# Kernel tuning notes

Measured on AMD Instinct MI355X. Metric: run time of the kernel, lower is better.

The kernel has to match this reference:

```python
import jax, jax.numpy as jnp
import numpy as np

PATCH_SIZE = 32
HALF = PATCH_SIZE // 2


def setup_inputs() -> dict:
    key = jax.random.key(0)
    k1, k2 = jax.random.split(key)
    B, L, H, W = 64, 106, 512, 512
    img = jax.random.normal(k1, (B, 1, H, W), dtype=jnp.float32)
    # landmarks are (x, y) pixel coords; uniform over the image
    landmarks = jax.random.uniform(k2, (B, L, 2), dtype=jnp.float32,
                                   minval=0.0, maxval=float(H - 1))
    return {"img": img, "landmarks": landmarks}


def reference(img, landmarks):
    B = landmarks.shape[0]
    H, W = img.shape[2], img.shape[3]
    # integer offset grid, K = (2*HALF+1)^2 entries of (o0, o1)
    r = jnp.arange(-HALF, HALF + 1, dtype=jnp.int32)
    oy, ox = jnp.meshgrid(r, r, indexing="ij")
    offsets = jnp.stack([oy.reshape(-1), ox.reshape(-1)], axis=-1)  # [K, 2] int32
    offsets_f = offsets.astype(jnp.float32)

    lm = jnp.clip(landmarks.reshape(B, -1, 2), float(HALF), float(H - 1 - HALF))  # [B,L,2]
    lm_long = jnp.floor(lm)  # coords are >= 0 so trunc == floor, matches .long()

    # integer pixel locations per (landmark, offset): [B, K, L, 2]
    loc = offsets[None, :, None, :] + lm_long[:, None, :, :].astype(jnp.int32)
    flat_idx = (loc[..., 0] + loc[..., 1] * W).reshape(B, -1)  # [B, K*L]

    # subpixel residual and splat weights
    dxdy = lm - lm_long  # [B, L, 2]
    sub = offsets_f[None, :, None, :] - dxdy[:, None, :, :]  # [B, K, L, 2]
    vals = (1.0 / (1.0 + jnp.sqrt(jnp.sum(sub * sub, axis=-1) + 1e-6))).reshape(B, -1)

    out = jnp.zeros((B, H * W), dtype=jnp.float32)
    out = out.at[jnp.arange(B)[:, None], flat_idx].add(vals)
    return out.reshape(B, 1, H, W)
```

## Files before the change

kernel.cpp:

```cpp
#include <hip/hip_runtime.h>

#define HALF 16
#define IMW  512
#define IMH  512
#define TILE 32
#define TPA  16
#define TPI  256
#define MAXL 256

typedef float f32x4 __attribute__((ext_vector_type(4)));

__global__ __launch_bounds__(256)
void lm_gather_kernel(const float* __restrict__ landmarks,
                      float* __restrict__ out,
                      int L)
{
    __shared__ float2 slm[MAXL];
    __shared__ int sn;

    const int t    = threadIdx.x;
    const int bx   = blockIdx.x;
    const int b    = bx >> 8;
    const int tile = bx & (TPI - 1);
    const int tx   = tile & (TPA - 1);
    const int ty   = tile >> 4;

    if (t == 0) sn = 0;
    __syncthreads();

    const float2* lmb = reinterpret_cast<const float2*>(landmarks) + (size_t)b * L;
    for (int j = t; j < L; j += 256) {
        float2 lm = lmb[j];
        float x0 = fminf(fmaxf(lm.x, (float)HALF), (float)(IMW - 1 - HALF));
        float x1 = fminf(fmaxf(lm.y, (float)HALF), (float)(IMH - 1 - HALF));
        int i0 = (int)x0;
        int i1 = (int)x1;
        int tx0 = (i0 - HALF) >> 5;
        int ty0 = (i1 - HALF) >> 5;
        if ((unsigned)(tx - tx0) <= 1u && (unsigned)(ty - ty0) <= 1u) {
            int pos = atomicAdd(&sn, 1);
            if (pos < MAXL) slm[pos] = make_float2(x0, x1);
        }
    }
    __syncthreads();
    const int n = min(sn, MAXL);

    const int py  = ty * TILE + (t >> 3);
    const int px0 = tx * TILE + (t & 7) * 4;
    const float fpy = (float)py;

    float acc[4] = {0.0f, 0.0f, 0.0f, 0.0f};
    for (int j = 0; j < n; ++j) {
        float2 e = slm[j];
        int   i0   = (int)e.x;
        int   i1   = (int)e.y;
        float dy   = fpy - e.y;
        float dy2e = dy * dy + 1e-6f;
        bool  in1  = (unsigned)(py - i1 + HALF) <= (unsigned)(2 * HALF);
        #pragma unroll
        for (int c = 0; c < 4; ++c) {
            int   px  = px0 + c;
            float dx  = (float)px - e.x;
            bool  in0 = (unsigned)(px - i0 + HALF) <= (unsigned)(2 * HALF);
            float v = __builtin_amdgcn_rcpf(1.0f + __builtin_amdgcn_sqrtf(dx * dx + dy2e));
            acc[c] += (in0 && in1) ? v : 0.0f;
        }
    }

    float* op = out + (size_t)b * (IMH * IMW) + (size_t)py * IMW + px0;
    f32x4 v4 = { acc[0], acc[1], acc[2], acc[3] };
    __builtin_nontemporal_store(v4, reinterpret_cast<f32x4*>(op));
}

extern "C" void kernel_launch(void* const* d_in, const int* in_sizes, int n_in,
                              void* d_out, int out_size, void* d_ws, size_t ws_size,
                              hipStream_t stream)
{
    const float* landmarks = (const float*)d_in[1];
    float* out = (float*)d_out;

    const int B = out_size / (IMH * IMW);
    const int L = in_sizes[1] / (2 * B);

    lm_gather_kernel<<<B * TPI, 256, 0, stream>>>(landmarks, out, L);
}
```

Baseline: 23.69 us.

## Process full-width row strips per block with binned landmarks and LDS-staged stores

Each block now handles a 32-row strip of the image instead of a 32x32 tile. Landmarks are scanned once per strip and binned into 16 column sub-tile lists, and results are staged in a 64KB shared buffer before being written out as contiguous rows. This aims to cut redundant landmark scanning and block-launch overhead. In exchange, occupancy is lower because of the large LDS use, the grid is much smaller, and compute is serialized before stores.

```diff
diff --git a/kernel.cpp b/kernel.cpp
--- a/kernel.cpp
+++ b/kernel.cpp
@@ -1,31 +1,31 @@
 #include <hip/hip_runtime.h>
 
-#define HALF 16
-#define IMW  512
-#define IMH  512
-#define TILE 32
-#define TPA  16
-#define TPI  256
-#define MAXL 256
+#define HALF   16
+#define IMW    512
+#define IMH    512
+#define SH     32
+#define NSTRIP (IMH / SH)
+#define NSUB   16
+#define CAP    64
 
 typedef float f32x4 __attribute__((ext_vector_type(4)));
 
 __global__ __launch_bounds__(256)
-void lm_gather_kernel(const float* __restrict__ landmarks,
-                      float* __restrict__ out,
-                      int L)
+void lm_strip_kernel(const float* __restrict__ landmarks,
+                     float* __restrict__ out,
+                     int L)
 {
-    __shared__ float2 slm[MAXL];
-    __shared__ int sn;
+    __shared__ float  sbuf[SH][IMW];
+    __shared__ float2 slist[NSUB][CAP];
+    __shared__ int    scnt[NSUB];
 
-    const int t    = threadIdx.x;
-    const int bx   = blockIdx.x;
-    const int b    = bx >> 8;
-    const int tile = bx & (TPI - 1);
-    const int tx   = tile & (TPA - 1);
-    const int ty   = tile >> 4;
+    const int t  = threadIdx.x;
+    const int bx = blockIdx.x;
+    const int b  = bx >> 4;
+    const int ty = bx & (NSTRIP - 1);
+    const int R  = ty * SH;
 
-    if (t == 0) sn = 0;
+    if (t < NSUB) scnt[t] = 0;
     __syncthreads();
 
     const float2* lmb = reinterpret_cast<const float2*>(landmarks) + (size_t)b * L;
@@ -35,41 +35,56 @@
         float x1 = fminf(fmaxf(lm.y, (float)HALF), (float)(IMH - 1 - HALF));
         int i0 = (int)x0;
         int i1 = (int)x1;
-        int tx0 = (i0 - HALF) >> 5;
-        int ty0 = (i1 - HALF) >> 5;
-        if ((unsigned)(tx - tx0) <= 1u && (unsigned)(ty - ty0) <= 1u) {
-            int pos = atomicAdd(&sn, 1);
-            if (pos < MAXL) slm[pos] = make_float2(x0, x1);
+        if ((unsigned)(i1 - (R - HALF)) < (unsigned)(SH + 2 * HALF)) {
+            int sx0 = (i0 - HALF) >> 5;
+            int sx1 = (i0 + HALF) >> 5;
+            int p0 = atomicAdd(&scnt[sx0], 1);
+            if (p0 < CAP) slist[sx0][p0] = make_float2(x0, x1);
+            if (sx1 != sx0) {
+                int p1 = atomicAdd(&scnt[sx1], 1);
+                if (p1 < CAP) slist[sx1][p1] = make_float2(x0, x1);
+            }
         }
     }
     __syncthreads();
-    const int n = min(sn, MAXL);
 
-    const int py  = ty * TILE + (t >> 3);
-    const int px0 = tx * TILE + (t & 7) * 4;
+    const int   r   = t >> 3;
+    const int   c0  = (t & 7) * 4;
+    const int   py  = R + r;
     const float fpy = (float)py;
 
-    float acc[4] = {0.0f, 0.0f, 0.0f, 0.0f};
-    for (int j = 0; j < n; ++j) {
-        float2 e = slm[j];
-        int   i0   = (int)e.x;
-        int   i1   = (int)e.y;
-        float dy   = fpy - e.y;
-        float dy2e = dy * dy + 1e-6f;
-        bool  in1  = (unsigned)(py - i1 + HALF) <= (unsigned)(2 * HALF);
-        #pragma unroll
-        for (int c = 0; c < 4; ++c) {
-            int   px  = px0 + c;
-            float dx  = (float)px - e.x;
-            bool  in0 = (unsigned)(px - i0 + HALF) <= (unsigned)(2 * HALF);
-            float v = __builtin_amdgcn_rcpf(1.0f + __builtin_amdgcn_sqrtf(dx * dx + dy2e));
-            acc[c] += (in0 && in1) ? v : 0.0f;
+    for (int tx = 0; tx < NSUB; ++tx) {
+        const int n   = min(scnt[tx], CAP);
+        const int px0 = tx * 32 + c0;
+        float acc[4] = {0.0f, 0.0f, 0.0f, 0.0f};
+        for (int j = 0; j < n; ++j) {
+            float2 e = slist[tx][j];
+            int   i0   = (int)e.x;
+            int   i1   = (int)e.y;
+            float dy   = fpy - e.y;
+            float dy2e = dy * dy + 1e-6f;
+            bool  in1  = (unsigned)(py - i1 + HALF) <= (unsigned)(2 * HALF);
+            #pragma unroll
+            for (int c = 0; c < 4; ++c) {
+                int   px  = px0 + c;
+                float dx  = (float)px - e.x;
+                bool  in0 = (unsigned)(px - i0 + HALF) <= (unsigned)(2 * HALF);
+                float v = __builtin_amdgcn_rcpf(1.0f + __builtin_amdgcn_sqrtf(dx * dx + dy2e));
+                acc[c] += (in0 && in1) ? v : 0.0f;
+            }
         }
+        f32x4 v4 = { acc[0], acc[1], acc[2], acc[3] };
+        *reinterpret_cast<f32x4*>(&sbuf[r][px0]) = v4;
     }
+    __syncthreads();
 
-    float* op = out + (size_t)b * (IMH * IMW) + (size_t)py * IMW + px0;
-    f32x4 v4 = { acc[0], acc[1], acc[2], acc[3] };
-    __builtin_nontemporal_store(v4, reinterpret_cast<f32x4*>(op));
+    float*       op = out + (size_t)b * (IMH * IMW) + (size_t)R * IMW;
+    const float* sp = &sbuf[0][0];
+    #pragma unroll
+    for (int s = 0; s < 16; ++s) {
+        f32x4 v = *reinterpret_cast<const f32x4*>(sp + s * 1024 + t * 4);
+        __builtin_nontemporal_store(v, reinterpret_cast<f32x4*>(op + s * 1024 + t * 4));
+    }
 }
 
 extern "C" void kernel_launch(void* const* d_in, const int* in_sizes, int n_in,
@@ -82,5 +97,5 @@
     const int B = out_size / (IMH * IMW);
     const int L = in_sizes[1] / (2 * B);
 
-    lm_gather_kernel<<<B * TPI, 256, 0, stream>>>(landmarks, out, L);
+    lm_strip_kernel<<<B * NSTRIP, 256, 0, stream>>>(landmarks, out, L);
 }
```

Measured after the change: 28.56 us. +20.6%, slower.

## Pre-bin landmarks per tile in a separate kernel before per-tile gather

Applied to the files above, without the earlier changes.

Adds a binning kernel, one block per image, that atomically appends each clamped landmark to the four 32x32 tile lists it can touch. The stored lists live in workspace with a per-tile cap of 48. The gather kernel then reads only its tile's short list instead of every block scanning all L landmarks and running a shared-memory atomic filter. It also replaces the nontemporal output store with a plain vector store. The cost is a second launch, a global-memory round trip, and a fixed cap: dense clusters past 48 entries would be silently truncated, where the old cap was 256.

```diff
diff --git a/kernel.cpp b/kernel.cpp
--- a/kernel.cpp
+++ b/kernel.cpp
@@ -3,55 +3,64 @@
 #define HALF 16
 #define IMW  512
 #define IMH  512
-#define TILE 32
-#define TPA  16
+#define TSZ  32
+#define NT   16
 #define TPI  256
-#define MAXL 256
+#define CAP  48
 
 typedef float f32x4 __attribute__((ext_vector_type(4)));
 
 __global__ __launch_bounds__(256)
-void lm_gather_kernel(const float* __restrict__ landmarks,
-                      float* __restrict__ out,
-                      int L)
+void lm_bin_kernel(const float* __restrict__ landmarks, int L,
+                   int* __restrict__ cnt, float2* __restrict__ lists)
 {
-    __shared__ float2 slm[MAXL];
-    __shared__ int sn;
-
-    const int t    = threadIdx.x;
-    const int bx   = blockIdx.x;
-    const int b    = bx >> 8;
-    const int tile = bx & (TPI - 1);
-    const int tx   = tile & (TPA - 1);
-    const int ty   = tile >> 4;
-
-    if (t == 0) sn = 0;
+    const int b = blockIdx.x;
+    const int t = threadIdx.x;
+    int* c = cnt + b * TPI;
+    if (t < TPI) c[t] = 0;
     __syncthreads();
-
-    const float2* lmb = reinterpret_cast<const float2*>(landmarks) + (size_t)b * L;
-    for (int j = t; j < L; j += 256) {
-        float2 lm = lmb[j];
+    if (t < L) {
+        float2 lm = reinterpret_cast<const float2*>(landmarks)[(size_t)b * L + t];
         float x0 = fminf(fmaxf(lm.x, (float)HALF), (float)(IMW - 1 - HALF));
         float x1 = fminf(fmaxf(lm.y, (float)HALF), (float)(IMH - 1 - HALF));
         int i0 = (int)x0;
         int i1 = (int)x1;
         int tx0 = (i0 - HALF) >> 5;
         int ty0 = (i1 - HALF) >> 5;
-        if ((unsigned)(tx - tx0) <= 1u && (unsigned)(ty - ty0) <= 1u) {
-            int pos = atomicAdd(&sn, 1);
-            if (pos < MAXL) slm[pos] = make_float2(x0, x1);
-        }
+        #pragma unroll
+        for (int dy = 0; dy < 2; ++dy)
+            #pragma unroll
+            for (int dx = 0; dx < 2; ++dx) {
+                int tile = (ty0 + dy) * NT + (tx0 + dx);
+                int pos = atomicAdd(&c[tile], 1);
+                if (pos < CAP)
+                    lists[((size_t)b * TPI + tile) * CAP + pos] = make_float2(x0, x1);
+            }
     }
-    __syncthreads();
-    const int n = min(sn, MAXL);
+}
 
-    const int py  = ty * TILE + (t >> 3);
-    const int px0 = tx * TILE + (t & 7) * 4;
+__global__ __launch_bounds__(256)
+void lm_gather_kernel(const int* __restrict__ cnt,
+                      const float2* __restrict__ lists,
+                      float* __restrict__ out)
+{
+    const int bx   = blockIdx.x;
+    const int b    = bx >> 8;
+    const int tile = bx & (TPI - 1);
+    const int tx   = tile & (NT - 1);
+    const int ty   = tile >> 4;
+
+    const int     n   = min(cnt[bx], CAP);
+    const float2* lst = lists + (size_t)bx * CAP;
+
+    const int   t   = threadIdx.x;
+    const int   py  = ty * TSZ + (t >> 3);
+    const int   px0 = tx * TSZ + (t & 7) * 4;
     const float fpy = (float)py;
 
     float acc[4] = {0.0f, 0.0f, 0.0f, 0.0f};
     for (int j = 0; j < n; ++j) {
-        float2 e = slm[j];
+        float2 e = lst[j];
         int   i0   = (int)e.x;
         int   i1   = (int)e.y;
         float dy   = fpy - e.y;
@@ -69,7 +78,7 @@
 
     float* op = out + (size_t)b * (IMH * IMW) + (size_t)py * IMW + px0;
     f32x4 v4 = { acc[0], acc[1], acc[2], acc[3] };
-    __builtin_nontemporal_store(v4, reinterpret_cast<f32x4*>(op));
+    *reinterpret_cast<f32x4*>(op) = v4;
 }
 
 extern "C" void kernel_launch(void* const* d_in, const int* in_sizes, int n_in,
@@ -82,5 +91,9 @@
     const int B = out_size / (IMH * IMW);
     const int L = in_sizes[1] / (2 * B);
 
-    lm_gather_kernel<<<B * TPI, 256, 0, stream>>>(landmarks, out, L);
+    int*    cnt   = (int*)d_ws;
+    float2* lists = (float2*)((char*)d_ws + (size_t)B * TPI * sizeof(int));
+
+    lm_bin_kernel<<<B, 256, 0, stream>>>(landmarks, L, cnt, lists);
+    lm_gather_kernel<<<B * TPI, 256, 0, stream>>>(cnt, lists, out);
 }
```

New measurement: 25.75 us. 8.7% more time.

## Process eight tiles per block with per-tile landmark lists from one scan

Applied to the files above, without the earlier changes.

Each block now covers a strip of eight 32x32 tiles instead of one, so the landmark array for a batch is scanned and binned once per strip rather than once per tile. Landmarks are binned into per-tile shared-memory lists capped at 48 entries. The grid shrinks eightfold, which lowers parallelism and lengthens each block's serial work. Output stores switch from nontemporal to normal stores. The cap of 48 could drop landmarks in dense tiles, though with uniform inputs that is unlikely.

```diff
diff --git a/kernel.cpp b/kernel.cpp
--- a/kernel.cpp
+++ b/kernel.cpp
@@ -3,29 +3,32 @@
 #define HALF 16
 #define IMW  512
 #define IMH  512
-#define TILE 32
-#define TPA  16
-#define TPI  256
-#define MAXL 256
+#define TSZ  32
+#define NT   16
+#define SPB  8
+#define BPI  32
+#define CAP  48
 
 typedef float f32x4 __attribute__((ext_vector_type(4)));
 
 __global__ __launch_bounds__(256)
-void lm_gather_kernel(const float* __restrict__ landmarks,
+void lm_strip8_kernel(const float* __restrict__ landmarks,
                       float* __restrict__ out,
                       int L)
 {
-    __shared__ float2 slm[MAXL];
-    __shared__ int sn;
+    __shared__ float2 slist[SPB][CAP];
+    __shared__ int    scnt[SPB];
 
-    const int t    = threadIdx.x;
-    const int bx   = blockIdx.x;
-    const int b    = bx >> 8;
-    const int tile = bx & (TPI - 1);
-    const int tx   = tile & (TPA - 1);
-    const int ty   = tile >> 4;
+    const int t   = threadIdx.x;
+    const int bx  = blockIdx.x;
+    const int b   = bx >> 5;
+    const int rem = bx & (BPI - 1);
+    const int ty  = rem >> 1;
+    const int tx0 = (rem & 1) * SPB;
+    const int R   = ty * TSZ;
+    const int C0  = tx0 * TSZ;
 
-    if (t == 0) sn = 0;
+    if (t < SPB) scnt[t] = 0;
     __syncthreads();
 
     const float2* lmb = reinterpret_cast<const float2*>(landmarks) + (size_t)b * L;
@@ -35,41 +38,48 @@
         float x1 = fminf(fmaxf(lm.y, (float)HALF), (float)(IMH - 1 - HALF));
         int i0 = (int)x0;
         int i1 = (int)x1;
-        int tx0 = (i0 - HALF) >> 5;
-        int ty0 = (i1 - HALF) >> 5;
-        if ((unsigned)(tx - tx0) <= 1u && (unsigned)(ty - ty0) <= 1u) {
-            int pos = atomicAdd(&sn, 1);
-            if (pos < MAXL) slm[pos] = make_float2(x0, x1);
+        if ((unsigned)(i1 - (R - HALF)) < (unsigned)(TSZ + 2 * HALF)) {
+            int g0 = (i0 - HALF) >> 5;
+            #pragma unroll
+            for (int d = 0; d < 2; ++d) {
+                int s = g0 + d - tx0;
+                if ((unsigned)s < (unsigned)SPB) {
+                    int pos = atomicAdd(&scnt[s], 1);
+                    if (pos < CAP) slist[s][pos] = make_float2(x0, x1);
+                }
+            }
         }
     }
     __syncthreads();
-    const int n = min(sn, MAXL);
 
-    const int py  = ty * TILE + (t >> 3);
-    const int px0 = tx * TILE + (t & 7) * 4;
+    const int   py  = R + (t >> 3);
+    const int   c4  = (t & 7) * 4;
     const float fpy = (float)py;
+    float* orow = out + (size_t)b * (IMH * IMW) + (size_t)py * IMW;
 
-    float acc[4] = {0.0f, 0.0f, 0.0f, 0.0f};
-    for (int j = 0; j < n; ++j) {
-        float2 e = slm[j];
-        int   i0   = (int)e.x;
-        int   i1   = (int)e.y;
-        float dy   = fpy - e.y;
-        float dy2e = dy * dy + 1e-6f;
-        bool  in1  = (unsigned)(py - i1 + HALF) <= (unsigned)(2 * HALF);
-        #pragma unroll
-        for (int c = 0; c < 4; ++c) {
-            int   px  = px0 + c;
-            float dx  = (float)px - e.x;
-            bool  in0 = (unsigned)(px - i0 + HALF) <= (unsigned)(2 * HALF);
-            float v = __builtin_amdgcn_rcpf(1.0f + __builtin_amdgcn_sqrtf(dx * dx + dy2e));
-            acc[c] += (in0 && in1) ? v : 0.0f;
+    for (int s = 0; s < SPB; ++s) {
+        const int n   = min(scnt[s], CAP);
+        const int px0 = C0 + s * TSZ + c4;
+        float acc[4] = {0.0f, 0.0f, 0.0f, 0.0f};
+        for (int j = 0; j < n; ++j) {
+            float2 e = slist[s][j];
+            int   i0   = (int)e.x;
+            int   i1   = (int)e.y;
+            float dy   = fpy - e.y;
+            float dy2e = dy * dy + 1e-6f;
+            bool  in1  = (unsigned)(py - i1 + HALF) <= (unsigned)(2 * HALF);
+            #pragma unroll
+            for (int c = 0; c < 4; ++c) {
+                int   px  = px0 + c;
+                float dx  = (float)px - e.x;
+                bool  in0 = (unsigned)(px - i0 + HALF) <= (unsigned)(2 * HALF);
+                float v = __builtin_amdgcn_rcpf(1.0f + __builtin_amdgcn_sqrtf(dx * dx + dy2e));
+                acc[c] += (in0 && in1) ? v : 0.0f;
+            }
         }
+        f32x4 v4 = { acc[0], acc[1], acc[2], acc[3] };
+        *reinterpret_cast<f32x4*>(orow + px0) = v4;
     }
-
-    float* op = out + (size_t)b * (IMH * IMW) + (size_t)py * IMW + px0;
-    f32x4 v4 = { acc[0], acc[1], acc[2], acc[3] };
-    __builtin_nontemporal_store(v4, reinterpret_cast<f32x4*>(op));
 }
 
 extern "C" void kernel_launch(void* const* d_in, const int* in_sizes, int n_in,
@@ -82,5 +92,5 @@
     const int B = out_size / (IMH * IMW);
     const int L = in_sizes[1] / (2 * B);
 
-    lm_gather_kernel<<<B * TPI, 256, 0, stream>>>(landmarks, out, L);
+    lm_strip8_kernel<<<B * BPI, 256, 0, stream>>>(landmarks, out, L);
 }
```

Measured after the change: 24.47 us. +3.3%, slower.
